# Optimization experiments

Measured on AMD Instinct MI355X. Metric: run time of the kernel, lower is better.

## Reference

```python
import jax, jax.numpy as jnp
import numpy as np

NPG = 2048               # nodes per graph (equal-sized graphs -> static topk)
KEEP_RATIO = 0.5
K = int(np.ceil(KEEP_RATIO * NPG))  # 1024 kept nodes per graph
N_NODES = 131072
N_EDGES = 2097152
D = 256


def setup_inputs() -> dict:
    key = jax.random.key(0)
    k1, k2, k3 = jax.random.split(key, 3)
    input_feature = jax.random.normal(k1, (N_NODES, D), dtype=jnp.float32)
    graph_indicator = (jnp.arange(N_NODES) // NPG).astype(jnp.int32)  # sorted, 64 graphs
    edge_index = jax.random.randint(k2, (2, N_EDGES), 0, N_NODES, dtype=jnp.int32)
    # GCNConv(D, 1) parameters
    W = jax.random.normal(k3, (D, 1), dtype=jnp.float32) / np.sqrt(D)
    b = jnp.zeros((1,), dtype=jnp.float32)
    return {"input_feature": input_feature, "graph_indicator": graph_indicator,
            "edge_index": edge_index, "W": W, "b": b}


def reference(input_feature, graph_indicator, edge_index, W, b):
    N, d = input_feature.shape
    B = N // NPG
    src, dst = edge_index[0], edge_index[1]
    # --- GCNConv(D -> 1): linear, add self-loops, symmetric norm, scatter-add ---
    h = input_feature @ W                      # [N, 1]
    loop = jnp.arange(N, dtype=edge_index.dtype)
    src2 = jnp.concatenate([src, loop])
    dst2 = jnp.concatenate([dst, loop])
    deg = jax.ops.segment_sum(jnp.ones_like(dst2, dtype=h.dtype), dst2, num_segments=N)
    dinv = jnp.where(deg > 0, deg ** -0.5, 0.0)
    norm = dinv[src2] * dinv[dst2]             # [E+N]
    attn = jax.ops.segment_sum(h[src2, 0] * norm, dst2, num_segments=N) + b[0]  # [N]
    # --- per-graph topk (keep_ratio), PyG order: descending score per graph ---
    s2d = attn.reshape(B, NPG)
    _, idx = jax.lax.top_k(s2d, K)             # [B, K] local indices
    perm = (idx + (jnp.arange(B, dtype=idx.dtype)[:, None] * NPG)).reshape(-1)  # [B*K]
    # --- gate kept features by tanh(score) ---
    new_x = input_feature[perm] * jnp.tanh(attn[perm])[:, None]   # [B*K, D]
    new_gi = graph_indicator[perm]
    # --- filter_adj: keep edges with both endpoints kept; remap ids; invalid -> -1 ---
    keep = jnp.zeros((N,), dtype=bool).at[perm].set(True)
    newid = jnp.full((N,), -1, dtype=edge_index.dtype).at[perm].set(
        jnp.arange(B * K, dtype=edge_index.dtype))
    emask = keep[src] & keep[dst]
    new_src = jnp.where(emask, newid[src], -1)
    new_dst = jnp.where(emask, newid[dst], -1)
    new_edge_index = jnp.stack([new_src, new_dst])  # [2, E], dropped edges marked -1
    return new_x, new_edge_index, new_gi
```

## Files before the change

kernel.cpp:

```cpp
#include <hip/hip_runtime.h>

#define NPG     2048
#define KKEEP   1024
#define NNODES  131072
#define NEDGES  2097152
#define DFEAT   256
#define NGRAPH  64
#define NKEPT   (NGRAPH * KKEEP)

#define NBLK    256
#define SLICE   (NEDGES / NBLK)
#define NBUCK   1024
#define BNODES  (NNODES / NBUCK)

__global__ __launch_bounds__(256) void k_dot_rows(const float* __restrict__ X,
                                                  const float* __restrict__ W,
                                                  float* __restrict__ h) {
    const int wave = threadIdx.x >> 6;
    const int lane = threadIdx.x & 63;
    const int row  = blockIdx.x * 4 + wave;
    const float4 x = *reinterpret_cast<const float4*>(X + (size_t)row * DFEAT + lane * 4);
    const float4 w = *reinterpret_cast<const float4*>(W + lane * 4);
    float v = x.x * w.x + x.y * w.y + x.z * w.z + x.w * w.w;
    #pragma unroll
    for (int off = 32; off; off >>= 1) v += __shfl_down(v, off, 64);
    if (lane == 0) h[row] = v;
}

__global__ __launch_bounds__(256) void k_binsort(const int* __restrict__ src,
                                                 const int* __restrict__ dst,
                                                 int* __restrict__ codes,
                                                 int* __restrict__ base) {
    __shared__ int hist[NBUCK];
    __shared__ int scan[256];
    __shared__ int lcode[SLICE];
    const int blk = blockIdx.x;
    const int t   = threadIdx.x;

    for (int i = t; i < NBUCK; i += 256) hist[i] = 0;
    __syncthreads();

    const int4* d4 = reinterpret_cast<const int4*>(dst) + blk * (SLICE / 4);
    const int4* s4 = reinterpret_cast<const int4*>(src) + blk * (SLICE / 4);

    for (int k = t; k < SLICE / 4; k += 256) {
        const int4 d = d4[k];
        atomicAdd(&hist[d.x >> 7], 1);
        atomicAdd(&hist[d.y >> 7], 1);
        atomicAdd(&hist[d.z >> 7], 1);
        atomicAdd(&hist[d.w >> 7], 1);
    }
    __syncthreads();

    const int v0 = hist[4 * t], v1 = hist[4 * t + 1],
              v2 = hist[4 * t + 2], v3 = hist[4 * t + 3];
    const int tsum = v0 + v1 + v2 + v3;
    scan[t] = tsum;
    __syncthreads();
    for (int off = 1; off < 256; off <<= 1) {
        const int x = (t >= off) ? scan[t - off] : 0;
        __syncthreads();
        scan[t] += x;
        __syncthreads();
    }
    const int excl = scan[t] - tsum;
    const int e0 = excl, e1 = e0 + v0, e2 = e1 + v1, e3 = e2 + v2;
    hist[4 * t]     = e0;
    hist[4 * t + 1] = e1;
    hist[4 * t + 2] = e2;
    hist[4 * t + 3] = e3;
    int4 eb; eb.x = e0; eb.y = e1; eb.z = e2; eb.w = e3;
    reinterpret_cast<int4*>(base + (size_t)blk * NBUCK)[t] = eb;
    __syncthreads();

    for (int k = t; k < SLICE / 4; k += 256) {
        const int4 d = d4[k];
        const int4 s = s4[k];
        int p;
        p = atomicAdd(&hist[d.x >> 7], 1); lcode[p] = ((d.x & 127) << 17) | s.x;
        p = atomicAdd(&hist[d.y >> 7], 1); lcode[p] = ((d.y & 127) << 17) | s.y;
        p = atomicAdd(&hist[d.z >> 7], 1); lcode[p] = ((d.z & 127) << 17) | s.z;
        p = atomicAdd(&hist[d.w >> 7], 1); lcode[p] = ((d.w & 127) << 17) | s.w;
    }
    __syncthreads();

    int4* out4 = reinterpret_cast<int4*>(codes) + blk * (SLICE / 4);
    for (int k = t; k < SLICE / 4; k += 256)
        out4[k] = reinterpret_cast<const int4*>(lcode)[k];
}

__global__ __launch_bounds__(256) void k_deg2(const int* __restrict__ codes,
                                              const int* __restrict__ base,
                                              int* __restrict__ deg) {
    __shared__ int acc[BNODES];
    const int b = blockIdx.x;
    const int t = threadIdx.x;
    if (t < BNODES) acc[t] = 0;
    __syncthreads();
    const int s0 = base[(size_t)t * NBUCK + b];
    const int s1 = (b == NBUCK - 1) ? SLICE : base[(size_t)t * NBUCK + b + 1];
    const int* c = codes + (size_t)t * SLICE;
    for (int k = s0; k < s1; ++k) atomicAdd(&acc[c[k] >> 17], 1);
    __syncthreads();
    if (t < BNODES) deg[b * BNODES + t] = acc[t];
}

__global__ __launch_bounds__(256) void k_prep(const int* __restrict__ deg,
                                              const float* __restrict__ h,
                                              float* __restrict__ dinv,
                                              float* __restrict__ g) {
    const int i = blockIdx.x * blockDim.x + threadIdx.x;
    const float di = 1.0f / sqrtf((float)(deg[i] + 1));
    dinv[i] = di;
    g[i] = h[i] * di;
}

__global__ __launch_bounds__(256) void k_attn(const int* __restrict__ codes,
                                              const int* __restrict__ base,
                                              const float* __restrict__ g,
                                              const float* __restrict__ dinv,
                                              const float* __restrict__ bias,
                                              float* __restrict__ attn) {
    __shared__ float acc[BNODES];
    const int b = blockIdx.x;
    const int t = threadIdx.x;
    if (t < BNODES) acc[t] = 0.0f;
    __syncthreads();
    const int s0 = base[(size_t)t * NBUCK + b];
    const int s1 = (b == NBUCK - 1) ? SLICE : base[(size_t)t * NBUCK + b + 1];
    const int* c = codes + (size_t)t * SLICE;
    for (int k = s0; k < s1; ++k) {
        const int code = c[k];
        atomicAdd(&acc[code >> 17], g[code & 0x1FFFF]);
    }
    __syncthreads();
    if (t < BNODES) {
        const int node = b * BNODES + t;
        attn[node] = (acc[t] + g[node]) * dinv[node] + bias[0];
    }
}

__global__ __launch_bounds__(256) void k_topk(const float* __restrict__ attn,
                                              int* __restrict__ perm,
                                              int* __restrict__ newid) {
    __shared__ unsigned long long key[NPG];
    __shared__ int pc[4][512];
    const int g = blockIdx.x >> 2;
    const int q = blockIdx.x & 3;
    const int t = threadIdx.x;
    const int wave = t >> 6;
    const int lane = t & 63;

    const float4* a4 = reinterpret_cast<const float4*>(attn + (size_t)g * NPG);
    for (int k4 = t; k4 < NPG / 4; k4 += 256) {
        const float4 v = a4[k4];
        const int j = k4 * 4;
        #pragma unroll
        for (int e = 0; e < 4; ++e) {
            const float f = (e == 0) ? v.x : (e == 1) ? v.y : (e == 2) ? v.z : v.w;
            unsigned int u = __float_as_uint(f);
            unsigned int m = (u & 0x80000000u) ? ~u : (u | 0x80000000u);
            key[j + e] = ((unsigned long long)m << 11) | (unsigned)(NPG - 1 - (j + e));
        }
    }
    __syncthreads();

    unsigned long long ki[8];
    int c[8];
    #pragma unroll
    for (int r = 0; r < 8; ++r) {
        ki[r] = key[q * 512 + r * 64 + lane];
        c[r] = 0;
    }

    const ulonglong2* k2 = reinterpret_cast<const ulonglong2*>(key) + wave * 256;
    #pragma unroll 4
    for (int k = 0; k < 256; ++k) {
        const ulonglong2 kk = k2[k];
        #pragma unroll
        for (int r = 0; r < 8; ++r) {
            c[r] += (int)(kk.x > ki[r]);
            c[r] += (int)(kk.y > ki[r]);
        }
    }
    #pragma unroll
    for (int r = 0; r < 8; ++r) pc[wave][r * 64 + lane] = c[r];
    __syncthreads();

    #pragma unroll
    for (int e = 0; e < 2; ++e) {
        const int il = e * 256 + t;
        const int rank = pc[0][il] + pc[1][il] + pc[2][il] + pc[3][il];
        const int node = g * NPG + q * 512 + il;
        if (rank < KKEEP) {
            const int id = g * KKEEP + rank;
            perm[id] = node;
            newid[node] = id;
        } else {
            newid[node] = -1;
        }
    }
}

__global__ __launch_bounds__(256) void k_gather(const float* __restrict__ X,
                                                const float* __restrict__ attn,
                                                const int* __restrict__ perm,
                                                float* __restrict__ out_x,
                                                float* __restrict__ out_gi) {
    const int wave = threadIdx.x >> 6;
    const int lane = threadIdx.x & 63;
    const int row  = blockIdx.x * 4 + wave;
    const int node = perm[row];
    const float gate = tanhf(attn[node]);
    const float4 x = *reinterpret_cast<const float4*>(X + (size_t)node * DFEAT + lane * 4);
    float4 o;
    o.x = x.x * gate; o.y = x.y * gate; o.z = x.z * gate; o.w = x.w * gate;
    *reinterpret_cast<float4*>(out_x + (size_t)row * DFEAT + lane * 4) = o;
    if (lane == 0) out_gi[row] = (float)(row >> 10);
}

__global__ __launch_bounds__(256) void k_edges(const int* __restrict__ src,
                                               const int* __restrict__ dst,
                                               const int* __restrict__ newid,
                                               float* __restrict__ out_src,
                                               float* __restrict__ out_dst) {
    const int i = blockIdx.x * blockDim.x + threadIdx.x;
    const int4 s = reinterpret_cast<const int4*>(src)[i];
    const int4 d = reinterpret_cast<const int4*>(dst)[i];
    const int ns0 = newid[s.x], nd0 = newid[d.x];
    const int ns1 = newid[s.y], nd1 = newid[d.y];
    const int ns2 = newid[s.z], nd2 = newid[d.z];
    const int ns3 = newid[s.w], nd3 = newid[d.w];
    float4 os, od;
    os.x = (ns0 >= 0 && nd0 >= 0) ? (float)ns0 : -1.0f;
    od.x = (ns0 >= 0 && nd0 >= 0) ? (float)nd0 : -1.0f;
    os.y = (ns1 >= 0 && nd1 >= 0) ? (float)ns1 : -1.0f;
    od.y = (ns1 >= 0 && nd1 >= 0) ? (float)nd1 : -1.0f;
    os.z = (ns2 >= 0 && nd2 >= 0) ? (float)ns2 : -1.0f;
    od.z = (ns2 >= 0 && nd2 >= 0) ? (float)nd2 : -1.0f;
    os.w = (ns3 >= 0 && nd3 >= 0) ? (float)ns3 : -1.0f;
    od.w = (ns3 >= 0 && nd3 >= 0) ? (float)nd3 : -1.0f;
    reinterpret_cast<float4*>(out_src)[i] = os;
    reinterpret_cast<float4*>(out_dst)[i] = od;
}

extern "C" void kernel_launch(void* const* d_in, const int* in_sizes, int n_in,
                              void* d_out, int out_size, void* d_ws, size_t ws_size,
                              hipStream_t stream) {
    const float* X  = (const float*)d_in[0];
    const int*   ei = (const int*)d_in[2];
    const float* W  = (const float*)d_in[3];
    const float* b  = (const float*)d_in[4];
    const int* src = ei;
    const int* dst = ei + NEDGES;

    char* ws = (char*)d_ws;
    int*   deg   = (int*)  (ws + 0 * (size_t)NNODES * 4);
    float* attn  = (float*)(ws + 1 * (size_t)NNODES * 4);
    float* h     = (float*)(ws + 2 * (size_t)NNODES * 4);
    float* dinv  = (float*)(ws + 3 * (size_t)NNODES * 4);
    float* gg    = (float*)(ws + 4 * (size_t)NNODES * 4);
    int*   newid = (int*)  (ws + 5 * (size_t)NNODES * 4);
    int*   perm  = (int*)  (ws + 6 * (size_t)NNODES * 4);

    float* out_x   = (float*)d_out;
    float* out_src = out_x + (size_t)NKEPT * DFEAT;
    float* out_dst = out_src + NEDGES;
    float* out_gi  = out_dst + NEDGES;

    int* codes = (int*)out_src;
    int* base  = (int*)out_dst;

    k_dot_rows<<<NNODES / 4, 256, 0, stream>>>(X, W, h);
    k_binsort <<<NBLK, 256, 0, stream>>>(src, dst, codes, base);
    k_deg2    <<<NBUCK, 256, 0, stream>>>(codes, base, deg);
    k_prep    <<<NNODES / 256, 256, 0, stream>>>(deg, h, dinv, gg);
    k_attn    <<<NBUCK, 256, 0, stream>>>(codes, base, gg, dinv, b, attn);
    k_topk    <<<NGRAPH * 4, 256, 0, stream>>>(attn, perm, newid);
    k_gather  <<<NKEPT / 4, 256, 0, stream>>>(X, attn, perm, out_x, out_gi);
    k_edges   <<<NEDGES / 4 / 256, 256, 0, stream>>>(src, dst, newid, out_src, out_dst);
}
```

Measured before the change: 342.7 us.

## Merge independent kernels into horizontally fused launches to cut launch count

Runs the row dot-product alongside the edge bin-sort in one launch, putting them in disjoint block ranges. Folds the degree-to-dinv prep into the degree-counting kernel, and merges the feature gather with the edge remap into a single launch. Dot and gather blocks now process 16 rows each instead of 4. The aim is fewer launches and serial gaps, and letting independent memory-bound work overlap on the GPU. The fused kernels share one LDS footprint sized by the bin-sort, which may limit occupancy for the dot-product blocks.

Measured after the change: 332.8 us. 1.03x faster.

```diff
diff --git a/kernel.cpp b/kernel.cpp
--- a/kernel.cpp
+++ b/kernel.cpp
@@ -13,85 +13,99 @@
 #define NBUCK   1024
 #define BNODES  (NNODES / NBUCK)
 
-__global__ __launch_bounds__(256) void k_dot_rows(const float* __restrict__ X,
-                                                  const float* __restrict__ W,
-                                                  float* __restrict__ h) {
-    const int wave = threadIdx.x >> 6;
-    const int lane = threadIdx.x & 63;
-    const int row  = blockIdx.x * 4 + wave;
-    const float4 x = *reinterpret_cast<const float4*>(X + (size_t)row * DFEAT + lane * 4);
-    const float4 w = *reinterpret_cast<const float4*>(W + lane * 4);
-    float v = x.x * w.x + x.y * w.y + x.z * w.z + x.w * w.w;
-    #pragma unroll
-    for (int off = 32; off; off >>= 1) v += __shfl_down(v, off, 64);
-    if (lane == 0) h[row] = v;
-}
-
-__global__ __launch_bounds__(256) void k_binsort(const int* __restrict__ src,
-                                                 const int* __restrict__ dst,
-                                                 int* __restrict__ codes,
-                                                 int* __restrict__ base) {
+#define DROWS   16
+#define DOTBLKS (NNODES / DROWS)
+#define GROWS   16
+#define GATBLKS (NKEPT / GROWS)
+#define EDGBLKS (NEDGES / 4 / 256)
+
+__global__ __launch_bounds__(256) void k_stage1(const float* __restrict__ X,
+                                                const float* __restrict__ W,
+                                                float* __restrict__ h,
+                                                const int* __restrict__ src,
+                                                const int* __restrict__ dst,
+                                                int* __restrict__ codes,
+                                                int* __restrict__ base) {
     __shared__ int hist[NBUCK];
-    __shared__ int scan[256];
+    __shared__ int scanb[256];
     __shared__ int lcode[SLICE];
-    const int blk = blockIdx.x;
-    const int t   = threadIdx.x;
-
-    for (int i = t; i < NBUCK; i += 256) hist[i] = 0;
-    __syncthreads();
-
-    const int4* d4 = reinterpret_cast<const int4*>(dst) + blk * (SLICE / 4);
-    const int4* s4 = reinterpret_cast<const int4*>(src) + blk * (SLICE / 4);
-
-    for (int k = t; k < SLICE / 4; k += 256) {
-        const int4 d = d4[k];
-        atomicAdd(&hist[d.x >> 7], 1);
-        atomicAdd(&hist[d.y >> 7], 1);
-        atomicAdd(&hist[d.z >> 7], 1);
-        atomicAdd(&hist[d.w >> 7], 1);
-    }
-    __syncthreads();
-
-    const int v0 = hist[4 * t], v1 = hist[4 * t + 1],
-              v2 = hist[4 * t + 2], v3 = hist[4 * t + 3];
-    const int tsum = v0 + v1 + v2 + v3;
-    scan[t] = tsum;
-    __syncthreads();
-    for (int off = 1; off < 256; off <<= 1) {
-        const int x = (t >= off) ? scan[t - off] : 0;
-        __syncthreads();
-        scan[t] += x;
-        __syncthreads();
-    }
-    const int excl = scan[t] - tsum;
-    const int e0 = excl, e1 = e0 + v0, e2 = e1 + v1, e3 = e2 + v2;
-    hist[4 * t]     = e0;
-    hist[4 * t + 1] = e1;
-    hist[4 * t + 2] = e2;
-    hist[4 * t + 3] = e3;
-    int4 eb; eb.x = e0; eb.y = e1; eb.z = e2; eb.w = e3;
-    reinterpret_cast<int4*>(base + (size_t)blk * NBUCK)[t] = eb;
-    __syncthreads();
-
-    for (int k = t; k < SLICE / 4; k += 256) {
-        const int4 d = d4[k];
-        const int4 s = s4[k];
-        int p;
-        p = atomicAdd(&hist[d.x >> 7], 1); lcode[p] = ((d.x & 127) << 17) | s.x;
-        p = atomicAdd(&hist[d.y >> 7], 1); lcode[p] = ((d.y & 127) << 17) | s.y;
-        p = atomicAdd(&hist[d.z >> 7], 1); lcode[p] = ((d.z & 127) << 17) | s.z;
-        p = atomicAdd(&hist[d.w >> 7], 1); lcode[p] = ((d.w & 127) << 17) | s.w;
-    }
-    __syncthreads();
-
-    int4* out4 = reinterpret_cast<int4*>(codes) + blk * (SLICE / 4);
-    for (int k = t; k < SLICE / 4; k += 256)
-        out4[k] = reinterpret_cast<const int4*>(lcode)[k];
-}
-
-__global__ __launch_bounds__(256) void k_deg2(const int* __restrict__ codes,
-                                              const int* __restrict__ base,
-                                              int* __restrict__ deg) {
+    const int t = threadIdx.x;
+
+    if (blockIdx.x < NBLK) {
+        const int blk = blockIdx.x;
+        for (int i = t; i < NBUCK; i += 256) hist[i] = 0;
+        __syncthreads();
+
+        const int4* d4 = reinterpret_cast<const int4*>(dst) + blk * (SLICE / 4);
+        const int4* s4 = reinterpret_cast<const int4*>(src) + blk * (SLICE / 4);
+
+        for (int k = t; k < SLICE / 4; k += 256) {
+            const int4 d = d4[k];
+            atomicAdd(&hist[d.x >> 7], 1);
+            atomicAdd(&hist[d.y >> 7], 1);
+            atomicAdd(&hist[d.z >> 7], 1);
+            atomicAdd(&hist[d.w >> 7], 1);
+        }
+        __syncthreads();
+
+        const int v0 = hist[4 * t], v1 = hist[4 * t + 1],
+                  v2 = hist[4 * t + 2], v3 = hist[4 * t + 3];
+        const int tsum = v0 + v1 + v2 + v3;
+        scanb[t] = tsum;
+        __syncthreads();
+        for (int off = 1; off < 256; off <<= 1) {
+            const int x = (t >= off) ? scanb[t - off] : 0;
+            __syncthreads();
+            scanb[t] += x;
+            __syncthreads();
+        }
+        const int excl = scanb[t] - tsum;
+        const int e0 = excl, e1 = e0 + v0, e2 = e1 + v1, e3 = e2 + v2;
+        hist[4 * t]     = e0;
+        hist[4 * t + 1] = e1;
+        hist[4 * t + 2] = e2;
+        hist[4 * t + 3] = e3;
+        int4 eb; eb.x = e0; eb.y = e1; eb.z = e2; eb.w = e3;
+        reinterpret_cast<int4*>(base + (size_t)blk * NBUCK)[t] = eb;
+        __syncthreads();
+
+        for (int k = t; k < SLICE / 4; k += 256) {
+            const int4 d = d4[k];
+            const int4 s = s4[k];
+            int p;
+            p = atomicAdd(&hist[d.x >> 7], 1); lcode[p] = ((d.x & 127) << 17) | s.x;
+            p = atomicAdd(&hist[d.y >> 7], 1); lcode[p] = ((d.y & 127) << 17) | s.y;
+            p = atomicAdd(&hist[d.z >> 7], 1); lcode[p] = ((d.z & 127) << 17) | s.z;
+            p = atomicAdd(&hist[d.w >> 7], 1); lcode[p] = ((d.w & 127) << 17) | s.w;
+        }
+        __syncthreads();
+
+        int4* out4 = reinterpret_cast<int4*>(codes) + blk * (SLICE / 4);
+        for (int k = t; k < SLICE / 4; k += 256)
+            out4[k] = reinterpret_cast<const int4*>(lcode)[k];
+    } else {
+        const int bid  = blockIdx.x - NBLK;
+        const int wave = t >> 6;
+        const int lane = t & 63;
+        const float4 w = *reinterpret_cast<const float4*>(W + lane * 4);
+        const int row0 = bid * DROWS + wave * (DROWS / 4);
+        #pragma unroll
+        for (int r = 0; r < DROWS / 4; ++r) {
+            const int row = row0 + r;
+            const float4 x = *reinterpret_cast<const float4*>(X + (size_t)row * DFEAT + lane * 4);
+            float v = x.x * w.x + x.y * w.y + x.z * w.z + x.w * w.w;
+            #pragma unroll
+            for (int off = 32; off; off >>= 1) v += __shfl_down(v, off, 64);
+            if (lane == 0) h[row] = v;
+        }
+    }
+}
+
+__global__ __launch_bounds__(256) void k_degprep(const int* __restrict__ codes,
+                                                 const int* __restrict__ base,
+                                                 const float* __restrict__ h,
+                                                 float* __restrict__ dinv,
+                                                 float* __restrict__ g) {
     __shared__ int acc[BNODES];
     const int b = blockIdx.x;
     const int t = threadIdx.x;
@@ -102,17 +116,12 @@
     const int* c = codes + (size_t)t * SLICE;
     for (int k = s0; k < s1; ++k) atomicAdd(&acc[c[k] >> 17], 1);
     __syncthreads();
-    if (t < BNODES) deg[b * BNODES + t] = acc[t];
-}
-
-__global__ __launch_bounds__(256) void k_prep(const int* __restrict__ deg,
-                                              const float* __restrict__ h,
-                                              float* __restrict__ dinv,
-                                              float* __restrict__ g) {
-    const int i = blockIdx.x * blockDim.x + threadIdx.x;
-    const float di = 1.0f / sqrtf((float)(deg[i] + 1));
-    dinv[i] = di;
-    g[i] = h[i] * di;
+    if (t < BNODES) {
+        const int node = b * BNODES + t;
+        const float di = 1.0f / sqrtf((float)(acc[t] + 1));
+        dinv[node] = di;
+        g[node] = h[node] * di;
+    }
 }
 
 __global__ __launch_bounds__(256) void k_attn(const int* __restrict__ codes,
@@ -202,46 +211,52 @@
     }
 }
 
-__global__ __launch_bounds__(256) void k_gather(const float* __restrict__ X,
+__global__ __launch_bounds__(256) void k_stage5(const float* __restrict__ X,
                                                 const float* __restrict__ attn,
                                                 const int* __restrict__ perm,
+                                                const int* __restrict__ newid,
+                                                const int* __restrict__ src,
+                                                const int* __restrict__ dst,
                                                 float* __restrict__ out_x,
-                                                float* __restrict__ out_gi) {
-    const int wave = threadIdx.x >> 6;
-    const int lane = threadIdx.x & 63;
-    const int row  = blockIdx.x * 4 + wave;
-    const int node = perm[row];
-    const float gate = tanhf(attn[node]);
-    const float4 x = *reinterpret_cast<const float4*>(X + (size_t)node * DFEAT + lane * 4);
-    float4 o;
-    o.x = x.x * gate; o.y = x.y * gate; o.z = x.z * gate; o.w = x.w * gate;
-    *reinterpret_cast<float4*>(out_x + (size_t)row * DFEAT + lane * 4) = o;
-    if (lane == 0) out_gi[row] = (float)(row >> 10);
-}
-
-__global__ __launch_bounds__(256) void k_edges(const int* __restrict__ src,
-                                               const int* __restrict__ dst,
-                                               const int* __restrict__ newid,
-                                               float* __restrict__ out_src,
-                                               float* __restrict__ out_dst) {
-    const int i = blockIdx.x * blockDim.x + threadIdx.x;
-    const int4 s = reinterpret_cast<const int4*>(src)[i];
-    const int4 d = reinterpret_cast<const int4*>(dst)[i];
-    const int ns0 = newid[s.x], nd0 = newid[d.x];
-    const int ns1 = newid[s.y], nd1 = newid[d.y];
-    const int ns2 = newid[s.z], nd2 = newid[d.z];
-    const int ns3 = newid[s.w], nd3 = newid[d.w];
-    float4 os, od;
-    os.x = (ns0 >= 0 && nd0 >= 0) ? (float)ns0 : -1.0f;
-    od.x = (ns0 >= 0 && nd0 >= 0) ? (float)nd0 : -1.0f;
-    os.y = (ns1 >= 0 && nd1 >= 0) ? (float)ns1 : -1.0f;
-    od.y = (ns1 >= 0 && nd1 >= 0) ? (float)nd1 : -1.0f;
-    os.z = (ns2 >= 0 && nd2 >= 0) ? (float)ns2 : -1.0f;
-    od.z = (ns2 >= 0 && nd2 >= 0) ? (float)nd2 : -1.0f;
-    os.w = (ns3 >= 0 && nd3 >= 0) ? (float)ns3 : -1.0f;
-    od.w = (ns3 >= 0 && nd3 >= 0) ? (float)nd3 : -1.0f;
-    reinterpret_cast<float4*>(out_src)[i] = os;
-    reinterpret_cast<float4*>(out_dst)[i] = od;
+                                                float* __restrict__ out_gi,
+                                                float* __restrict__ out_src,
+                                                float* __restrict__ out_dst) {
+    if (blockIdx.x < EDGBLKS) {
+        const int i = blockIdx.x * 256 + threadIdx.x;
+        const int4 s = reinterpret_cast<const int4*>(src)[i];
+        const int4 d = reinterpret_cast<const int4*>(dst)[i];
+        const int ns0 = newid[s.x], nd0 = newid[d.x];
+        const int ns1 = newid[s.y], nd1 = newid[d.y];
+        const int ns2 = newid[s.z], nd2 = newid[d.z];
+        const int ns3 = newid[s.w], nd3 = newid[d.w];
+        float4 os, od;
+        os.x = (ns0 >= 0 && nd0 >= 0) ? (float)ns0 : -1.0f;
+        od.x = (ns0 >= 0 && nd0 >= 0) ? (float)nd0 : -1.0f;
+        os.y = (ns1 >= 0 && nd1 >= 0) ? (float)ns1 : -1.0f;
+        od.y = (ns1 >= 0 && nd1 >= 0) ? (float)nd1 : -1.0f;
+        os.z = (ns2 >= 0 && nd2 >= 0) ? (float)ns2 : -1.0f;
+        od.z = (ns2 >= 0 && nd2 >= 0) ? (float)nd2 : -1.0f;
+        os.w = (ns3 >= 0 && nd3 >= 0) ? (float)ns3 : -1.0f;
+        od.w = (ns3 >= 0 && nd3 >= 0) ? (float)nd3 : -1.0f;
+        reinterpret_cast<float4*>(out_src)[i] = os;
+        reinterpret_cast<float4*>(out_dst)[i] = od;
+    } else {
+        const int bid  = blockIdx.x - EDGBLKS;
+        const int wave = threadIdx.x >> 6;
+        const int lane = threadIdx.x & 63;
+        const int row0 = bid * GROWS + wave * (GROWS / 4);
+        #pragma unroll
+        for (int r = 0; r < GROWS / 4; ++r) {
+            const int row  = row0 + r;
+            const int node = perm[row];
+            const float gate = tanhf(attn[node]);
+            const float4 x = *reinterpret_cast<const float4*>(X + (size_t)node * DFEAT + lane * 4);
+            float4 o;
+            o.x = x.x * gate; o.y = x.y * gate; o.z = x.z * gate; o.w = x.w * gate;
+            *reinterpret_cast<float4*>(out_x + (size_t)row * DFEAT + lane * 4) = o;
+            if (lane == 0) out_gi[row] = (float)(row >> 10);
+        }
+    }
 }
 
 extern "C" void kernel_launch(void* const* d_in, const int* in_sizes, int n_in,
@@ -255,13 +270,12 @@
     const int* dst = ei + NEDGES;
 
     char* ws = (char*)d_ws;
-    int*   deg   = (int*)  (ws + 0 * (size_t)NNODES * 4);
-    float* attn  = (float*)(ws + 1 * (size_t)NNODES * 4);
-    float* h     = (float*)(ws + 2 * (size_t)NNODES * 4);
-    float* dinv  = (float*)(ws + 3 * (size_t)NNODES * 4);
-    float* gg    = (float*)(ws + 4 * (size_t)NNODES * 4);
-    int*   newid = (int*)  (ws + 5 * (size_t)NNODES * 4);
-    int*   perm  = (int*)  (ws + 6 * (size_t)NNODES * 4);
+    float* attn  = (float*)(ws + 0 * (size_t)NNODES * 4);
+    float* h     = (float*)(ws + 1 * (size_t)NNODES * 4);
+    float* dinv  = (float*)(ws + 2 * (size_t)NNODES * 4);
+    float* gg    = (float*)(ws + 3 * (size_t)NNODES * 4);
+    int*   newid = (int*)  (ws + 4 * (size_t)NNODES * 4);
+    int*   perm  = (int*)  (ws + 5 * (size_t)NNODES * 4);
 
     float* out_x   = (float*)d_out;
     float* out_src = out_x + (size_t)NKEPT * DFEAT;
@@ -271,12 +285,10 @@
     int* codes = (int*)out_src;
     int* base  = (int*)out_dst;
 
-    k_dot_rows<<<NNODES / 4, 256, 0, stream>>>(X, W, h);
-    k_binsort <<<NBLK, 256, 0, stream>>>(src, dst, codes, base);
-    k_deg2    <<<NBUCK, 256, 0, stream>>>(codes, base, deg);
-    k_prep    <<<NNODES / 256, 256, 0, stream>>>(deg, h, dinv, gg);
-    k_attn    <<<NBUCK, 256, 0, stream>>>(codes, base, gg, dinv, b, attn);
-    k_topk    <<<NGRAPH * 4, 256, 0, stream>>>(attn, perm, newid);
-    k_gather  <<<NKEPT / 4, 256, 0, stream>>>(X, attn, perm, out_x, out_gi);
-    k_edges   <<<NEDGES / 4 / 256, 256, 0, stream>>>(src, dst, newid, out_src, out_dst);
-}
+    k_stage1 <<<NBLK + DOTBLKS, 256, 0, stream>>>(X, W, h, src, dst, codes, base);
+    k_degprep<<<NBUCK, 256, 0, stream>>>(codes, base, h, dinv, gg);
+    k_attn   <<<NBUCK, 256, 0, stream>>>(codes, base, gg, dinv, b, attn);
+    k_topk   <<<NGRAPH * 4, 256, 0, stream>>>(attn, perm, newid);
+    k_stage5 <<<EDGBLKS + GATBLKS, 256, 0, stream>>>(X, attn, perm, newid, src, dst,
+                                                     out_x, out_gi, out_src, out_dst);
+}
```
